# Optimization experiments

Measured on AMD Instinct MI355X. Metric: run time of the kernel, lower is better.

Reference implementation:

```python
import jax, jax.numpy as jnp
import numpy as np

N, E, F_NODE, F_EDGE, HID, B, GDIM, ACT = 50000, 1600000, 32, 8, 256, 64, 16, 64
N_HIDDEN_LAYERS = 3


def setup_inputs() -> dict:
    key = jax.random.key(0)
    ks = jax.random.split(key, 16)
    x = jax.random.normal(ks[0], (N, F_NODE), jnp.float32)
    edge_index = jax.random.randint(ks[1], (2, E), 0, N, jnp.int64)
    edge_attr = jax.random.normal(ks[2], (E, F_EDGE), jnp.float32)
    batch = jnp.sort(jax.random.randint(ks[3], (N,), 0, B, jnp.int64))
    global_feats = jax.random.normal(ks[4], (B, GDIM), jnp.float32)
    s = lambda *d: 1.0 / np.sqrt(d[-2])
    # layer 0: node_feat -> hidden ; layers 1..3: hidden -> hidden
    We0 = jax.random.normal(ks[5], (F_EDGE, F_NODE), jnp.float32) * (1.0 / np.sqrt(F_EDGE))
    W0 = jax.random.normal(ks[6], (F_NODE, HID), jnp.float32) * (1.0 / np.sqrt(F_NODE))
    b0 = jnp.zeros((HID,), jnp.float32)
    We = jax.random.normal(ks[7], (N_HIDDEN_LAYERS, F_EDGE, HID), jnp.float32) * (1.0 / np.sqrt(F_EDGE))
    W = jax.random.normal(ks[8], (N_HIDDEN_LAYERS, HID, HID), jnp.float32) * (1.0 / np.sqrt(HID))
    b = jnp.zeros((N_HIDDEN_LAYERS, HID), jnp.float32)
    Wp = jax.random.normal(ks[9], (HID + GDIM, ACT), jnp.float32) * (1.0 / np.sqrt(HID + GDIM))
    bp = jnp.zeros((ACT,), jnp.float32)
    Wv = jax.random.normal(ks[10], (HID + GDIM, 1), jnp.float32) * (1.0 / np.sqrt(HID + GDIM))
    bv = jnp.zeros((1,), jnp.float32)
    return {"x": x, "edge_attr": edge_attr, "global_feats": global_feats,
            "We0": We0, "W0": W0, "b0": b0, "We": We, "W": W, "b": b,
            "Wp": Wp, "bp": bp, "Wv": Wv, "bv": bv,
            "edge_index": edge_index, "batch": batch}


def reference(x, edge_attr, global_feats, We0, W0, b0, We, W, b, Wp, bp, Wv, bv, edge_index, batch):
    src, dst = edge_index[0], edge_index[1]
    n_nodes = x.shape[0]
    n_graphs = global_feats.shape[0]

    def conv(h, We_l, W_l, b_l):
        # GINE-style: message relu(x_j + proj(e_ij)), sum-aggregate, node update MLP
        m = jax.nn.relu(h[src] + edge_attr @ We_l)            # [E, d]
        agg = jax.ops.segment_sum(m, dst, num_segments=n_nodes)
        return jax.nn.relu((h + agg) @ W_l + b_l)             # [N, hidden]

    h = conv(x, We0, W0, b0)
    for i in range(We.shape[0]):
        h = conv(h, We[i], W[i], b[i])

    counts = jax.ops.segment_sum(jnp.ones((n_nodes, 1), h.dtype), batch, num_segments=n_graphs)
    pooled = jax.ops.segment_sum(h, batch, num_segments=n_graphs) / jnp.maximum(counts, 1.0)
    feats = jnp.concatenate([pooled, global_feats], axis=-1)  # [B, hidden+gdim]
    logits = feats @ Wp + bp                                  # [B, max_action_dim]
    value = feats @ Wv + bv                                   # [B, 1]
    return logits, value
```

## Files before the change

kernel.cpp:

```cpp
#include <hip/hip_runtime.h>
#include <hip/hip_bf16.h>

#define NNODES 50000
#define NEDGES 1600000
#define FNODE 32
#define FEDGE 8
#define HIDD 256
#define NGRAPH 64
#define GDIM 16
#define NACT 64
#define FEATD (HIDD + GDIM)
#define PCH 8

typedef short bf16x8 __attribute__((ext_vector_type(8)));
typedef float f32x4 __attribute__((ext_vector_type(4)));
typedef __bf16 bf16x2 __attribute__((ext_vector_type(2)));


__device__ inline float bfl(uint u) {
  union { uint i; float f; } v; v.i = u << 16; return v.f;
}
__device__ inline float bfh(uint u) {
  union { uint i; float f; } v; v.i = u & 0xffff0000u; return v.f;
}
__device__ inline float bf1(ushort u) {
  union { uint i; float f; } v; v.i = ((uint)u) << 16; return v.f;
}
__device__ inline ushort f2b(float a) {
  __hip_bfloat16 h = __float2bfloat16(a);
  return *(ushort*)&h;
}
__device__ inline uint packbf(float a, float b) {
  return (uint)f2b(a) | ((uint)f2b(b) << 16);
}

__device__ inline float dot2bf(uint a, uint b, float c) {
#if defined(__has_builtin)
#if __has_builtin(__builtin_amdgcn_fdot2_f32_bf16)
  union { uint u; bf16x2 v; } ua, ub;
  ua.u = a; ub.u = b;
  return __builtin_amdgcn_fdot2_f32_bf16(ua.v, ub.v, c, false);
#else
  return fmaf(bfl(a), bfl(b), fmaf(bfh(a), bfh(b), c));
#endif
#else
  return fmaf(bfl(a), bfl(b), fmaf(bfh(a), bfh(b), c));
#endif
}


__global__ void k_zero_i32(int* __restrict__ p, int n) {
  int i = blockIdx.x * blockDim.x + threadIdx.x;
  if (i < n) p[i] = 0;
}

__global__ void k_hist(const int* __restrict__ dst, int* __restrict__ off) {
  int e = blockIdx.x * blockDim.x + threadIdx.x;
  if (e < NEDGES) atomicAdd(&off[dst[e] + 1], 1);
}

__global__ void k_scan1(int* __restrict__ data, int n, int* __restrict__ sums) {
  __shared__ int buf[1024];
  int gid = blockIdx.x * 1024 + threadIdx.x;
  int v = (gid < n) ? data[gid] : 0;
  buf[threadIdx.x] = v;
  __syncthreads();
  for (int d = 1; d < 1024; d <<= 1) {
    int t = (threadIdx.x >= d) ? buf[threadIdx.x - d] : 0;
    __syncthreads();
    buf[threadIdx.x] += t;
    __syncthreads();
  }
  if (gid < n) data[gid] = buf[threadIdx.x];
  if (threadIdx.x == 1023) sums[blockIdx.x] = buf[1023];
}

__global__ void k_scan3(int* __restrict__ data, int n, const int* __restrict__ sums,
                        int* __restrict__ cur) {
  int base = 0;
  for (int i = 0; i < (int)blockIdx.x; ++i) base += sums[i];
  int gid = blockIdx.x * 1024 + threadIdx.x;
  if (gid < n) {
    int v = data[gid] + base;
    data[gid] = v;
    if (gid < NNODES) cur[gid] = v;
  }
}

__global__ void k_scatter(const int* __restrict__ src, const int* __restrict__ dst,
                          int* __restrict__ cur, const float* __restrict__ ea,
                          int* __restrict__ csr_src, ushort* __restrict__ eab) {
  int e = blockIdx.x * blockDim.x + threadIdx.x;
  if (e >= NEDGES) return;
  int d = dst[e];
  int pos = atomicAdd(&cur[d], 1);
  csr_src[pos] = src[e];
  float4 a = *(const float4*)&ea[(size_t)e * FEDGE];
  float4 b = *(const float4*)&ea[(size_t)e * FEDGE + 4];
  uint4 o;
  o.x = packbf(a.x, a.y);
  o.y = packbf(a.z, a.w);
  o.z = packbf(b.x, b.y);
  o.w = packbf(b.z, b.w);
  *(uint4*)&eab[(size_t)pos * FEDGE] = o;
}


#define CVT_N (NNODES * FNODE / 4)
#define WEP_N (128 + 3 * 1024)
#define WP_N (1024 + 3 * 8192)

__global__ void k_prep(const float* __restrict__ x, ushort* __restrict__ xb,
                       const float* __restrict__ We0, const float* __restrict__ We,
                       uint* __restrict__ wep0, uint* __restrict__ wep,
                       const float* __restrict__ W0, const float* __restrict__ W,
                       ushort* __restrict__ wp0, ushort* __restrict__ wp) {
  int i = blockIdx.x * blockDim.x + threadIdx.x;
  if (i < CVT_N) {
    float4 v = *(const float4*)&x[(size_t)i * 4];
    uint2 o;
    o.x = packbf(v.x, v.y);
    o.y = packbf(v.z, v.w);
    *(uint2*)&xb[(size_t)i * 4] = o;
    return;
  }
  i -= CVT_N;
  if (i < WEP_N) {
    if (i < 128) {
      int k2 = i >> 5, c = i & 31;
      wep0[i] = packbf(We0[(2 * k2) * FNODE + c], We0[(2 * k2 + 1) * FNODE + c]);
    } else {
      int u = i - 128;
      int l = u >> 10;
      int r = u & 1023;
      int k2 = r >> 8, c = r & 255;
      const float* Wl = We + (size_t)l * FEDGE * HIDD;
      wep[u] = packbf(Wl[(2 * k2) * HIDD + c], Wl[(2 * k2 + 1) * HIDD + c]);
    }
    return;
  }
  i -= WEP_N;
  if (i < WP_N) {
    if (i < 1024) {
      int lane = i & 63;
      int nf = i >> 6;
      int col = nf * 16 + (lane & 15);
      int k0 = (lane >> 4) * 8;
      ushort o[8];
#pragma unroll
      for (int q = 0; q < 8; ++q) o[q] = f2b(W0[(size_t)(k0 + q) * HIDD + col]);
      *(uint4*)&wp0[(size_t)i * 8] = *(uint4*)o;
    } else {
      int u = i - 1024;
      int l = u / 8192;
      int r = u - l * 8192;
      int lane = r & 63;
      int frag = r >> 6;
      int nf = frag & 15, ks = frag >> 4;
      int col = nf * 16 + (lane & 15);
      int k0 = ks * 32 + (lane >> 4) * 8;
      const float* Wl = W + (size_t)l * HIDD * HIDD;
      ushort o[8];
#pragma unroll
      for (int q = 0; q < 8; ++q) o[q] = f2b(Wl[(size_t)(k0 + q) * HIDD + col]);
      *(uint4*)&wp[(size_t)u * 8] = *(uint4*)o;
    }
  }
}


__global__ __launch_bounds__(256) void k_edge32(
    const float* __restrict__ x, const ushort* __restrict__ xb,
    const uint4* __restrict__ eab4, const uint* __restrict__ wep0,
    const int* __restrict__ off, const int* __restrict__ csr_src,
    ushort* __restrict__ t0b) {
  int wid = __builtin_amdgcn_readfirstlane(
      (int)((blockIdx.x * blockDim.x + threadIdx.x) >> 6));
  if (wid >= NNODES) return;
  int lane = threadIdx.x & 63;
  int j = lane >> 5;
  int c = lane & 31;
  uint w0 = wep0[c], w1 = wep0[32 + c], w2 = wep0[64 + c], w3 = wep0[96 + c];
  int s0 = off[wid], s1 = off[wid + 1];
  float acc = 0.f;
  int e = s0 + j;
  for (; e + 6 < s1; e += 8) {
    int sA = csr_src[e], sB = csr_src[e + 2], sC = csr_src[e + 4], sD = csr_src[e + 6];
    ushort hA = xb[(size_t)sA * FNODE + c];
    ushort hB = xb[(size_t)sB * FNODE + c];
    ushort hC = xb[(size_t)sC * FNODE + c];
    ushort hD = xb[(size_t)sD * FNODE + c];
    uint4 eA = eab4[e];
    uint4 eB = eab4[e + 2];
    uint4 eC = eab4[e + 4];
    uint4 eD = eab4[e + 6];
    float pr;
#define B32(hu, eu)                 \
    pr = bf1(hu);                   \
    pr = dot2bf(eu.x, w0, pr);      \
    pr = dot2bf(eu.y, w1, pr);      \
    pr = dot2bf(eu.z, w2, pr);      \
    pr = dot2bf(eu.w, w3, pr);      \
    acc += fmaxf(pr, 0.f);
    B32(hA, eA) B32(hB, eB) B32(hC, eC) B32(hD, eD)
  }
  for (; e < s1; e += 2) {
    int s = csr_src[e];
    ushort hu = xb[(size_t)s * FNODE + c];
    uint4 eu = eab4[e];
    float pr;
    B32(hu, eu)
#undef B32
  }
  acc += __shfl_xor(acc, 32);
  if (j == 0) t0b[wid * FNODE + c] = f2b(x[wid * FNODE + c] + acc);
}


__device__ inline void body_dot(uint2 hu, uint4 eu, const uint4 wq[4], float4& acc) {
  float4 pr;
  pr.x = bfl(hu.x);
  pr.y = bfh(hu.x);
  pr.z = bfl(hu.y);
  pr.w = bfh(hu.y);
  pr.x = dot2bf(eu.x, wq[0].x, pr.x);
  pr.x = dot2bf(eu.y, wq[1].x, pr.x);
  pr.x = dot2bf(eu.z, wq[2].x, pr.x);
  pr.x = dot2bf(eu.w, wq[3].x, pr.x);
  pr.y = dot2bf(eu.x, wq[0].y, pr.y);
  pr.y = dot2bf(eu.y, wq[1].y, pr.y);
  pr.y = dot2bf(eu.z, wq[2].y, pr.y);
  pr.y = dot2bf(eu.w, wq[3].y, pr.y);
  pr.z = dot2bf(eu.x, wq[0].z, pr.z);
  pr.z = dot2bf(eu.y, wq[1].z, pr.z);
  pr.z = dot2bf(eu.z, wq[2].z, pr.z);
  pr.z = dot2bf(eu.w, wq[3].z, pr.z);
  pr.w = dot2bf(eu.x, wq[0].w, pr.w);
  pr.w = dot2bf(eu.y, wq[1].w, pr.w);
  pr.w = dot2bf(eu.z, wq[2].w, pr.w);
  pr.w = dot2bf(eu.w, wq[3].w, pr.w);
  acc.x += fmaxf(pr.x, 0.f);
  acc.y += fmaxf(pr.y, 0.f);
  acc.z += fmaxf(pr.z, 0.f);
  acc.w += fmaxf(pr.w, 0.f);
}

#define EDGE_BLOCK(U)                                                       \
  for (; e + (U) <= s1; e += (U)) {                                         \
    int s[U];                                                               \
    uint2 h[U];                                                             \
    uint4 E[U];                                                             \
    _Pragma("unroll") for (int u = 0; u < (U); ++u) s[u] = csr_src[e + u];  \
    _Pragma("unroll") for (int u = 0; u < (U); ++u)                         \
        h[u] = *(const uint2*)&hb[(size_t)s[u] * HIDD + c];                 \
    _Pragma("unroll") for (int u = 0; u < (U); ++u) E[u] = eab4[e + u];     \
    _Pragma("unroll") for (int u = 0; u < (U); ++u)                         \
        body_dot(h[u], E[u], wq, (u & 1) ? acc1 : acc0);                    \
  }

__global__ __launch_bounds__(256) void k_edge256(
    const ushort* __restrict__ hb, const uint4* __restrict__ eab4,
    const uint* __restrict__ wepl, const int* __restrict__ off,
    const int* __restrict__ csr_src, ushort* __restrict__ tb) {
  int wid = __builtin_amdgcn_readfirstlane(
      (int)((blockIdx.x * blockDim.x + threadIdx.x) >> 6));
  if (wid >= NNODES) return;
  int lane = threadIdx.x & 63;
  int c = lane * 4;
  uint4 wq[4];
#pragma unroll
  for (int k2 = 0; k2 < 4; ++k2) wq[k2] = *(const uint4*)&wepl[k2 * HIDD + c];
  int s0 = off[wid], s1 = off[wid + 1];
  float4 acc0 = {0.f, 0.f, 0.f, 0.f}, acc1 = {0.f, 0.f, 0.f, 0.f};
  int e = s0;
  EDGE_BLOCK(16)
  EDGE_BLOCK(8)
  EDGE_BLOCK(4)
  for (; e < s1; ++e) {
    int s = csr_src[e];
    uint2 hu = *(const uint2*)&hb[(size_t)s * HIDD + c];
    uint4 eu = eab4[e];
    body_dot(hu, eu, wq, acc0);
  }

  uint2 su = *(const uint2*)&hb[(size_t)wid * HIDD + c];
  float4 o;
  o.x = bfl(su.x) + acc0.x + acc1.x;
  o.y = bfh(su.x) + acc0.y + acc1.y;
  o.z = bfl(su.y) + acc0.z + acc1.z;
  o.w = bfh(su.y) + acc0.w + acc1.w;
  uint2 ob;
  ob.x = packbf(o.x, o.y);
  ob.y = packbf(o.z, o.w);
  *(uint2*)&tb[(size_t)wid * HIDD + c] = ob;
}
#undef EDGE_BLOCK


template <int K>
__global__ __launch_bounds__(512) void k_gemm_mfma(
    const ushort* __restrict__ Tb, const ushort* __restrict__ Wp,
    const float* __restrict__ bias, ushort* __restrict__ outb, int nrows) {
  constexpr int KS = K / 32;
  constexpr int KSH = (KS >= 4) ? 4 : KS;
  constexpr int CH = KSH * 16 * 64;
  __shared__ ushort bl[CH * 8];
  const int tid = threadIdx.x;
  const int wave = tid >> 6;
  const int lane = tid & 63;
  const int row0 = blockIdx.x * 128 + wave * 16;
  const int arow = row0 + (lane & 15);
  const int kgrp = lane >> 4;
  f32x4 acc[16];
#pragma unroll
  for (int nf = 0; nf < 16; ++nf) acc[nf] = (f32x4){0.f, 0.f, 0.f, 0.f};
#pragma unroll
  for (int st = 0; st < KS / KSH; ++st) {
    __syncthreads();
    for (int chk = tid; chk < CH; chk += 512)
      *(uint4*)&bl[(size_t)chk * 8] = *(const uint4*)&Wp[((size_t)st * CH + chk) * 8];
    __syncthreads();
#pragma unroll
    for (int ksl = 0; ksl < KSH; ++ksl) {
      int ks = st * KSH + ksl;
      bf16x8 af = *(const bf16x8*)&Tb[(size_t)arow * K + ks * 32 + kgrp * 8];
#pragma unroll
      for (int nf = 0; nf < 16; ++nf) {
        bf16x8 bfg = *(const bf16x8*)&bl[((size_t)(ksl * 16 + nf) * 64 + lane) * 8];
        acc[nf] = __builtin_amdgcn_mfma_f32_16x16x32_bf16(af, bfg, acc[nf], 0, 0, 0);
      }
    }
  }
  const int ocol0 = lane & 15;
  const int orow0 = row0 + (lane >> 4) * 4;
#pragma unroll
  for (int nf = 0; nf < 16; ++nf) {
    int col = nf * 16 + ocol0;
    float bv = bias[col];
#pragma unroll
    for (int r = 0; r < 4; ++r) {
      int row = orow0 + r;
      if (row < nrows) outb[(size_t)row * HIDD + col] = f2b(fmaxf(acc[nf][r] + bv, 0.f));
    }
  }
}


__global__ void k_pool_partial(const ushort* __restrict__ hb, const int* __restrict__ batch,
                               float* __restrict__ fp) {
  int b = blockIdx.x >> 3;
  int j = blockIdx.x & 7;
  __shared__ int srange[2];
  if (threadIdx.x < 2) {
    int target = b + threadIdx.x;
    int lo = 0, hi = NNODES;
    while (lo < hi) {
      int mid = (lo + hi) >> 1;
      if (batch[mid] < target) lo = mid + 1; else hi = mid;
    }
    srange[threadIdx.x] = lo;
  }
  __syncthreads();
  int s = srange[0], eend = srange[1];
  int len = eend - s;
  int cs = s + (int)((long long)len * j / PCH);
  int ce = s + (int)((long long)len * (j + 1) / PCH);
  int col = threadIdx.x;
  float acc = 0.f;
  for (int n = cs; n < ce; ++n) acc += bf1(hb[(size_t)n * HIDD + col]);
  fp[((size_t)j * NGRAPH + b) * HIDD + col] = acc;
}

__global__ void k_pool_final(const float* __restrict__ fp, const int* __restrict__ batch,
                             const float* __restrict__ gf, float* __restrict__ feats) {
  int b = blockIdx.x;
  __shared__ int srange[2];
  if (threadIdx.x < 2) {
    int target = b + threadIdx.x;
    int lo = 0, hi = NNODES;
    while (lo < hi) {
      int mid = (lo + hi) >> 1;
      if (batch[mid] < target) lo = mid + 1; else hi = mid;
    }
    srange[threadIdx.x] = lo;
  }
  __syncthreads();
  int col = threadIdx.x;
  float acc = 0.f;
#pragma unroll
  for (int j = 0; j < PCH; ++j) acc += fp[((size_t)j * NGRAPH + b) * HIDD + col];
  float cnt = fmaxf((float)(srange[1] - srange[0]), 1.0f);
  feats[b * FEATD + col] = acc / cnt;
  if (col < GDIM) feats[b * FEATD + HIDD + col] = gf[b * GDIM + col];
}


__global__ void k_heads(const float* __restrict__ feats, const float* __restrict__ Wp,
                        const float* __restrict__ bp, const float* __restrict__ Wv,
                        const float* __restrict__ bv, float* __restrict__ out) {
  int b = blockIdx.x;
  int t = threadIdx.x;
  __shared__ float f[FEATD];
  for (int i = t; i < FEATD; i += 64) f[i] = feats[b * FEATD + i];
  __syncthreads();
  float acc = bp[t];
  for (int k = 0; k < FEATD; ++k) acc = fmaf(f[k], Wp[k * NACT + t], acc);
  out[b * NACT + t] = acc;
  float pv = 0.f;
  for (int k = t; k < FEATD; k += 64) pv = fmaf(f[k], Wv[k], pv);
#pragma unroll
  for (int d = 32; d > 0; d >>= 1) pv += __shfl_down(pv, d);
  if (t == 0) out[NGRAPH * NACT + b] = pv + bv[0];
}


extern "C" void kernel_launch(void* const* d_in, const int* in_sizes, int n_in,
                              void* d_out, int out_size, void* d_ws, size_t ws_size,
                              hipStream_t stream) {
  const float* x   = (const float*)d_in[0];
  const float* ea  = (const float*)d_in[1];
  const float* gf  = (const float*)d_in[2];
  const float* We0 = (const float*)d_in[3];
  const float* W0  = (const float*)d_in[4];
  const float* b0  = (const float*)d_in[5];
  const float* We  = (const float*)d_in[6];
  const float* W   = (const float*)d_in[7];
  const float* bb  = (const float*)d_in[8];
  const float* Wp  = (const float*)d_in[9];
  const float* bp  = (const float*)d_in[10];
  const float* Wv  = (const float*)d_in[11];
  const float* bv  = (const float*)d_in[12];
  const int* eidx  = (const int*)d_in[13];
  const int* batch = (const int*)d_in[14];
  const int* esrc = eidx;
  const int* edst = eidx + NEDGES;

  char* w = (char*)d_ws;
  size_t p = 0;
  auto take = [&](size_t bytes) {
    size_t r = p;
    p += (bytes + 255) & ~(size_t)255;
    return r;
  };
  int* off      = (int*)(w + take((NNODES + 1) * 4));
  int* cur      = (int*)(w + take(NNODES * 4));
  int* sums     = (int*)(w + take(1024));
  int* csr_src  = (int*)(w + take((size_t)NEDGES * 4));
  ushort* eab   = (ushort*)(w + take((size_t)NEDGES * FEDGE * 2));
  ushort* t0b   = (ushort*)(w + take((size_t)NNODES * FNODE * 2));
  ushort* xb    = (ushort*)(w + take((size_t)NNODES * FNODE * 2));
  ushort* tb    = (ushort*)(w + take((size_t)NNODES * HIDD * 2));
  ushort* hb    = (ushort*)(w + take((size_t)NNODES * HIDD * 2));
  uint* wep0    = (uint*)(w + take(128 * 4));
  uint* wepb    = (uint*)(w + take(3 * 1024 * 4));
  ushort* wp0   = (ushort*)(w + take((size_t)1024 * 8 * 2));
  ushort* wpb   = (ushort*)(w + take((size_t)3 * 8192 * 8 * 2));
  float* fp     = (float*)(w + take((size_t)PCH * NGRAPH * HIDD * 4));
  float* feats  = (float*)(w + take((size_t)NGRAPH * FEATD * 4));
  if (p > ws_size) return;

  k_zero_i32<<<(NNODES + 1 + 255) / 256, 256, 0, stream>>>(off, NNODES + 1);
  k_hist<<<(NEDGES + 255) / 256, 256, 0, stream>>>(edst, off);
  int n_scan = NNODES + 1;
  int nb_scan = (n_scan + 1023) / 1024;
  k_scan1<<<nb_scan, 1024, 0, stream>>>(off, n_scan, sums);
  k_scan3<<<nb_scan, 1024, 0, stream>>>(off, n_scan, sums, cur);
  k_scatter<<<(NEDGES + 255) / 256, 256, 0, stream>>>(esrc, edst, cur, ea, csr_src, eab);

  k_prep<<<(CVT_N + WEP_N + WP_N + 255) / 256, 256, 0, stream>>>(
      x, xb, We0, We, wep0, wepb, W0, W, wp0, wpb);

  const int gemm_grid = (NNODES + 127) / 128;

  k_edge32<<<NNODES / 4, 256, 0, stream>>>(x, xb, (const uint4*)eab, wep0, off,
                                           csr_src, t0b);
  k_gemm_mfma<FNODE><<<gemm_grid, 512, 0, stream>>>(t0b, wp0, b0, hb, NNODES);

  for (int l = 0; l < 3; ++l) {
    k_edge256<<<NNODES / 4, 256, 0, stream>>>(hb, (const uint4*)eab, wepb + l * 1024,
                                              off, csr_src, tb);
    k_gemm_mfma<HIDD><<<gemm_grid, 512, 0, stream>>>(
        tb, wpb + (size_t)l * 8192 * 8, bb + (size_t)l * HIDD, hb, NNODES);
  }

  k_pool_partial<<<NGRAPH * PCH, HIDD, 0, stream>>>(hb, batch, fp);
  k_pool_final<<<NGRAPH, HIDD, 0, stream>>>(fp, batch, gf, feats);
  k_heads<<<NGRAPH, 64, 0, stream>>>(feats, Wp, bp, Wv, bv, (float*)d_out);
}
```

Measured before the change: 703.3 us.

## Pipeline edge gathers, prescale CSR indices, shrink GEMM blocks, fuse small kernels

CSR source indices are stored prescaled so the edge kernels compute gather addresses with 32-bit adds. The hidden-layer edge kernel becomes a double-buffered loop that loads the next 4-edge chunk while computing the current one. The GEMM moves from 512-thread, 128-row blocks to 256-thread, 64-row blocks with a smaller staged weight slice. The histogram is fused into the prep kernel, and pooling-final is fused with the heads, cutting launches and the feats buffer. The extra registers from double buffering may lower occupancy, and the smaller GEMM blocks reload weights more often.

```diff
diff --git a/kernel.cpp b/kernel.cpp
--- a/kernel.cpp
+++ b/kernel.cpp
@@ -54,11 +54,6 @@
   if (i < n) p[i] = 0;
 }
 
-__global__ void k_hist(const int* __restrict__ dst, int* __restrict__ off) {
-  int e = blockIdx.x * blockDim.x + threadIdx.x;
-  if (e < NEDGES) atomicAdd(&off[dst[e] + 1], 1);
-}
-
 __global__ void k_scan1(int* __restrict__ data, int n, int* __restrict__ sums) {
   __shared__ int buf[1024];
   int gid = blockIdx.x * 1024 + threadIdx.x;
@@ -94,7 +89,7 @@
   if (e >= NEDGES) return;
   int d = dst[e];
   int pos = atomicAdd(&cur[d], 1);
-  csr_src[pos] = src[e];
+  csr_src[pos] = src[e] * 64;
   float4 a = *(const float4*)&ea[(size_t)e * FEDGE];
   float4 b = *(const float4*)&ea[(size_t)e * FEDGE + 4];
   uint4 o;
@@ -110,12 +105,15 @@
 #define WEP_N (128 + 3 * 1024)
 #define WP_N (1024 + 3 * 8192)
 
-__global__ void k_prep(const float* __restrict__ x, ushort* __restrict__ xb,
-                       const float* __restrict__ We0, const float* __restrict__ We,
-                       uint* __restrict__ wep0, uint* __restrict__ wep,
-                       const float* __restrict__ W0, const float* __restrict__ W,
-                       ushort* __restrict__ wp0, ushort* __restrict__ wp) {
-  int i = blockIdx.x * blockDim.x + threadIdx.x;
+__global__ void k_hist_prep(const int* __restrict__ dst, int* __restrict__ off,
+                            const float* __restrict__ x, ushort* __restrict__ xb,
+                            const float* __restrict__ We0, const float* __restrict__ We,
+                            uint* __restrict__ wep0, uint* __restrict__ wep,
+                            const float* __restrict__ W0, const float* __restrict__ W,
+                            ushort* __restrict__ wp0, ushort* __restrict__ wp) {
+  int gid = blockIdx.x * blockDim.x + threadIdx.x;
+  if (gid < NEDGES) atomicAdd(&off[dst[gid] + 1], 1);
+  int i = gid;
   if (i < CVT_N) {
     float4 v = *(const float4*)&x[(size_t)i * 4];
     uint2 o;
@@ -180,16 +178,17 @@
   int lane = threadIdx.x & 63;
   int j = lane >> 5;
   int c = lane & 31;
+  uint c2 = (uint)c * 2;
+  const char* xbase = (const char*)xb;
   uint w0 = wep0[c], w1 = wep0[32 + c], w2 = wep0[64 + c], w3 = wep0[96 + c];
   int s0 = off[wid], s1 = off[wid + 1];
   float acc = 0.f;
   int e = s0 + j;
   for (; e + 6 < s1; e += 8) {
-    int sA = csr_src[e], sB = csr_src[e + 2], sC = csr_src[e + 4], sD = csr_src[e + 6];
-    ushort hA = xb[(size_t)sA * FNODE + c];
-    ushort hB = xb[(size_t)sB * FNODE + c];
-    ushort hC = xb[(size_t)sC * FNODE + c];
-    ushort hD = xb[(size_t)sD * FNODE + c];
+    ushort hA = *(const ushort*)(xbase + ((uint)csr_src[e] + c2));
+    ushort hB = *(const ushort*)(xbase + ((uint)csr_src[e + 2] + c2));
+    ushort hC = *(const ushort*)(xbase + ((uint)csr_src[e + 4] + c2));
+    ushort hD = *(const ushort*)(xbase + ((uint)csr_src[e + 6] + c2));
     uint4 eA = eab4[e];
     uint4 eB = eab4[e + 2];
     uint4 eC = eab4[e + 4];
@@ -205,8 +204,7 @@
     B32(hA, eA) B32(hB, eB) B32(hC, eC) B32(hD, eD)
   }
   for (; e < s1; e += 2) {
-    int s = csr_src[e];
-    ushort hu = xb[(size_t)s * FNODE + c];
+    ushort hu = *(const ushort*)(xbase + ((uint)csr_src[e] + c2));
     uint4 eu = eab4[e];
     float pr;
     B32(hu, eu)
@@ -245,18 +243,16 @@
   acc.w += fmaxf(pr.w, 0.f);
 }
 
-#define EDGE_BLOCK(U)                                                       \
-  for (; e + (U) <= s1; e += (U)) {                                         \
-    int s[U];                                                               \
-    uint2 h[U];                                                             \
-    uint4 E[U];                                                             \
-    _Pragma("unroll") for (int u = 0; u < (U); ++u) s[u] = csr_src[e + u];  \
-    _Pragma("unroll") for (int u = 0; u < (U); ++u)                         \
-        h[u] = *(const uint2*)&hb[(size_t)s[u] * HIDD + c];                 \
-    _Pragma("unroll") for (int u = 0; u < (U); ++u) E[u] = eab4[e + u];     \
-    _Pragma("unroll") for (int u = 0; u < (U); ++u)                         \
-        body_dot(h[u], E[u], wq, (u & 1) ? acc1 : acc0);                    \
-  }
+#define LOADCH(H, E_, eb)                                                   \
+  _Pragma("unroll") for (int u = 0; u < 4; ++u) {                           \
+    uint boff = ((uint)csr_src[(eb) + u] << 3) + c8;                        \
+    H[u] = *(const uint2*)(hbase + boff);                                   \
+  }                                                                         \
+  _Pragma("unroll") for (int u = 0; u < 4; ++u) E_[u] = eab4[(eb) + u];
+
+#define COMPCH(H, E_)                                                       \
+  _Pragma("unroll") for (int u = 0; u < 4; ++u)                             \
+    body_dot(H[u], E_[u], wq, (u & 1) ? acc1 : acc0);
 
 __global__ __launch_bounds__(256) void k_edge256(
     const ushort* __restrict__ hb, const uint4* __restrict__ eab4,
@@ -267,18 +263,40 @@
   if (wid >= NNODES) return;
   int lane = threadIdx.x & 63;
   int c = lane * 4;
+  uint c8 = (uint)lane * 8;
+  const char* hbase = (const char*)hb;
   uint4 wq[4];
 #pragma unroll
   for (int k2 = 0; k2 < 4; ++k2) wq[k2] = *(const uint4*)&wepl[k2 * HIDD + c];
   int s0 = off[wid], s1 = off[wid + 1];
   float4 acc0 = {0.f, 0.f, 0.f, 0.f}, acc1 = {0.f, 0.f, 0.f, 0.f};
   int e = s0;
-  EDGE_BLOCK(16)
-  EDGE_BLOCK(8)
-  EDGE_BLOCK(4)
+  int nch = (s1 - s0) >> 2;
+  if (nch > 0) {
+    uint2 hA[4], hB[4];
+    uint4 EA[4], EB[4];
+    LOADCH(hA, EA, e)
+    int t = 1;
+    for (; t + 1 < nch; t += 2) {
+      LOADCH(hB, EB, e + 4)
+      COMPCH(hA, EA)
+      LOADCH(hA, EA, e + 8)
+      COMPCH(hB, EB)
+      e += 8;
+    }
+    if (t < nch) {
+      LOADCH(hB, EB, e + 4)
+      COMPCH(hA, EA)
+      COMPCH(hB, EB)
+      e += 8;
+    } else {
+      COMPCH(hA, EA)
+      e += 4;
+    }
+  }
   for (; e < s1; ++e) {
-    int s = csr_src[e];
-    uint2 hu = *(const uint2*)&hb[(size_t)s * HIDD + c];
+    uint boff = ((uint)csr_src[e] << 3) + c8;
+    uint2 hu = *(const uint2*)(hbase + boff);
     uint4 eu = eab4[e];
     body_dot(hu, eu, wq, acc0);
   }
@@ -294,21 +312,22 @@
   ob.y = packbf(o.z, o.w);
   *(uint2*)&tb[(size_t)wid * HIDD + c] = ob;
 }
-#undef EDGE_BLOCK
+#undef LOADCH
+#undef COMPCH
 
 
 template <int K>
-__global__ __launch_bounds__(512) void k_gemm_mfma(
+__global__ __launch_bounds__(256) void k_gemm_mfma(
     const ushort* __restrict__ Tb, const ushort* __restrict__ Wp,
     const float* __restrict__ bias, ushort* __restrict__ outb, int nrows) {
   constexpr int KS = K / 32;
-  constexpr int KSH = (KS >= 4) ? 4 : KS;
+  constexpr int KSH = (KS >= 2) ? 2 : KS;
   constexpr int CH = KSH * 16 * 64;
   __shared__ ushort bl[CH * 8];
   const int tid = threadIdx.x;
   const int wave = tid >> 6;
   const int lane = tid & 63;
-  const int row0 = blockIdx.x * 128 + wave * 16;
+  const int row0 = blockIdx.x * 64 + wave * 16;
   const int arow = row0 + (lane & 15);
   const int kgrp = lane >> 4;
   f32x4 acc[16];
@@ -317,8 +336,11 @@
 #pragma unroll
   for (int st = 0; st < KS / KSH; ++st) {
     __syncthreads();
-    for (int chk = tid; chk < CH; chk += 512)
-      *(uint4*)&bl[(size_t)chk * 8] = *(const uint4*)&Wp[((size_t)st * CH + chk) * 8];
+#pragma unroll
+    for (int chk = 0; chk < CH / 256; ++chk) {
+      int ch = chk * 256 + tid;
+      *(uint4*)&bl[(size_t)ch * 8] = *(const uint4*)&Wp[((size_t)st * CH + ch) * 8];
+    }
     __syncthreads();
 #pragma unroll
     for (int ksl = 0; ksl < KSH; ++ksl) {
@@ -371,9 +393,13 @@
   fp[((size_t)j * NGRAPH + b) * HIDD + col] = acc;
 }
 
-__global__ void k_pool_final(const float* __restrict__ fp, const int* __restrict__ batch,
-                             const float* __restrict__ gf, float* __restrict__ feats) {
+
+__global__ void k_pool_heads(const float* __restrict__ fp, const int* __restrict__ batch,
+                             const float* __restrict__ gf, const float* __restrict__ Wp,
+                             const float* __restrict__ bp, const float* __restrict__ Wv,
+                             const float* __restrict__ bv, float* __restrict__ out) {
   int b = blockIdx.x;
+  __shared__ float f[FEATD];
   __shared__ int srange[2];
   if (threadIdx.x < 2) {
     int target = b + threadIdx.x;
@@ -390,27 +416,21 @@
 #pragma unroll
   for (int j = 0; j < PCH; ++j) acc += fp[((size_t)j * NGRAPH + b) * HIDD + col];
   float cnt = fmaxf((float)(srange[1] - srange[0]), 1.0f);
-  feats[b * FEATD + col] = acc / cnt;
-  if (col < GDIM) feats[b * FEATD + HIDD + col] = gf[b * GDIM + col];
-}
-
-
-__global__ void k_heads(const float* __restrict__ feats, const float* __restrict__ Wp,
-                        const float* __restrict__ bp, const float* __restrict__ Wv,
-                        const float* __restrict__ bv, float* __restrict__ out) {
-  int b = blockIdx.x;
-  int t = threadIdx.x;
-  __shared__ float f[FEATD];
-  for (int i = t; i < FEATD; i += 64) f[i] = feats[b * FEATD + i];
+  f[col] = acc / cnt;
+  if (col < GDIM) f[HIDD + col] = gf[b * GDIM + col];
   __syncthreads();
-  float acc = bp[t];
-  for (int k = 0; k < FEATD; ++k) acc = fmaf(f[k], Wp[k * NACT + t], acc);
-  out[b * NACT + t] = acc;
-  float pv = 0.f;
-  for (int k = t; k < FEATD; k += 64) pv = fmaf(f[k], Wv[k], pv);
-#pragma unroll
-  for (int d = 32; d > 0; d >>= 1) pv += __shfl_down(pv, d);
-  if (t == 0) out[NGRAPH * NACT + b] = pv + bv[0];
+  if (col < NACT) {
+    float lg = bp[col];
+    for (int k = 0; k < FEATD; ++k) lg = fmaf(f[k], Wp[k * NACT + col], lg);
+    out[b * NACT + col] = lg;
+  } else if (col < 128) {
+    int t = col - 64;
+    float pv = 0.f;
+    for (int k = t; k < FEATD; k += 64) pv = fmaf(f[k], Wv[k], pv);
+#pragma unroll
+    for (int d = 32; d > 0; d >>= 1) pv += __shfl_down(pv, d);
+    if (t == 0) out[NGRAPH * NACT + b] = pv + bv[0];
+  }
 }
 
 
@@ -456,34 +476,31 @@
   ushort* wp0   = (ushort*)(w + take((size_t)1024 * 8 * 2));
   ushort* wpb   = (ushort*)(w + take((size_t)3 * 8192 * 8 * 2));
   float* fp     = (float*)(w + take((size_t)PCH * NGRAPH * HIDD * 4));
-  float* feats  = (float*)(w + take((size_t)NGRAPH * FEATD * 4));
   if (p > ws_size) return;
 
   k_zero_i32<<<(NNODES + 1 + 255) / 256, 256, 0, stream>>>(off, NNODES + 1);
-  k_hist<<<(NEDGES + 255) / 256, 256, 0, stream>>>(edst, off);
+  k_hist_prep<<<(NEDGES + 255) / 256, 256, 0, stream>>>(
+      edst, off, x, xb, We0, We, wep0, wepb, W0, W, wp0, wpb);
   int n_scan = NNODES + 1;
   int nb_scan = (n_scan + 1023) / 1024;
   k_scan1<<<nb_scan, 1024, 0, stream>>>(off, n_scan, sums);
   k_scan3<<<nb_scan, 1024, 0, stream>>>(off, n_scan, sums, cur);
   k_scatter<<<(NEDGES + 255) / 256, 256, 0, stream>>>(esrc, edst, cur, ea, csr_src, eab);
 
-  k_prep<<<(CVT_N + WEP_N + WP_N + 255) / 256, 256, 0, stream>>>(
-      x, xb, We0, We, wep0, wepb, W0, W, wp0, wpb);
-
-  const int gemm_grid = (NNODES + 127) / 128;
+  const int gemm_grid = (NNODES + 63) / 64;
 
   k_edge32<<<NNODES / 4, 256, 0, stream>>>(x, xb, (const uint4*)eab, wep0, off,
                                            csr_src, t0b);
-  k_gemm_mfma<FNODE><<<gemm_grid, 512, 0, stream>>>(t0b, wp0, b0, hb, NNODES);
+  k_gemm_mfma<FNODE><<<gemm_grid, 256, 0, stream>>>(t0b, wp0, b0, hb, NNODES);
 
   for (int l = 0; l < 3; ++l) {
     k_edge256<<<NNODES / 4, 256, 0, stream>>>(hb, (const uint4*)eab, wepb + l * 1024,
                                               off, csr_src, tb);
-    k_gemm_mfma<HIDD><<<gemm_grid, 512, 0, stream>>>(
+    k_gemm_mfma<HIDD><<<gemm_grid, 256, 0, stream>>>(
         tb, wpb + (size_t)l * 8192 * 8, bb + (size_t)l * HIDD, hb, NNODES);
   }
 
   k_pool_partial<<<NGRAPH * PCH, HIDD, 0, stream>>>(hb, batch, fp);
-  k_pool_final<<<NGRAPH, HIDD, 0, stream>>>(fp, batch, gf, feats);
-  k_heads<<<NGRAPH, 64, 0, stream>>>(feats, Wp, bp, Wv, bv, (float*)d_out);
-}
+  k_pool_heads<<<NGRAPH, HIDD, 0, stream>>>(fp, batch, gf, Wp, bp, Wv, bv,
+                                            (float*)d_out);
+}
```

Result: no change. 692.7 us (-1.5%).
